# Performance work log

Hardware: AMD Instinct MI355X
Metric: run time of the kernel (lower is better)

Reference implementation:

```python
import jax, jax.numpy as jnp
import numpy as np

N = 50000      # nodes
K = 16         # neighbors per node (adj has K+1 cols; col 0 = self, sliced off)
NFEAT = 128
NHID = 128
NCLASS = 64
SLOPE = 0.2    # LeakyReLU slope used by Tail-GNN Relation module


def _relation(xg, mean_x, G1, G2, B1, B2, r):
    # xg: [N,K,F] gathered neighbor features, mean_x: [N,F] weighted mean
    # FiLM-style relation (TransE translation), mean-pooled over neighbors
    nb = (mean_x @ G2)[:, None, :]
    gamma = jax.nn.leaky_relu(jnp.einsum('nkf,fg->nkg', xg, G1) + nb, SLOPE) + 1.0
    nb2 = (mean_x @ B2)[:, None, :]
    beta = jax.nn.leaky_relu(jnp.einsum('nkf,fg->nkg', xg, B1) + nb2, SLOPE)
    r_v = gamma * r + beta                       # [N,K,F]
    return jnp.mean(xg + r_v - mean_x[:, None, :], axis=1)  # [N,F]


def _lrgcn(x, idx, w1, w2, W, G1, G2, B1, B2, r):
    nbr = idx[:, 1:]                              # [N,K] drop self column
    xg = x[nbr]                                   # [N,K,F] irregular gather
    mean_x = jnp.mean(xg * w1[:, 1:, None], axis=1)   # [N,F]
    m = _relation(xg, mean_x, G1, G2, B1, B2, r)      # [N,F]
    # tail=False branch: embed = mean_k(W(xg) * w2); W is linear (no bias)
    # so aggregate first, then transform (same math, less memory)
    embed = jnp.mean(xg * w2[:, 1:, None], axis=1) @ W  # [N,H]
    return embed, m


def setup_inputs() -> dict:
    key = jax.random.key(0)
    ks = jax.random.split(key, 20)
    s = 0.05
    inp = {
        'x': jax.random.normal(ks[0], (N, NFEAT), jnp.float32),
        'adj1_idx': jax.random.randint(ks[1], (N, K + 1), 0, N),
        'adj1_w1': jax.random.uniform(ks[2], (N, K + 1), jnp.float32),
        'adj1_w2': jax.random.uniform(ks[3], (N, K + 1), jnp.float32),
        'adj2_idx': jax.random.randint(ks[4], (N, K + 1), 0, N),
        'adj2_w1': jax.random.uniform(ks[5], (N, K + 1), jnp.float32),
        'adj2_w2': jax.random.uniform(ks[6], (N, K + 1), jnp.float32),
        'W1': jax.random.normal(ks[7], (NFEAT, NHID), jnp.float32) * s,
        'W2': jax.random.normal(ks[8], (NHID, NCLASS), jnp.float32) * s,
        'r1_G1': jax.random.normal(ks[9], (NFEAT, NFEAT), jnp.float32) * s,
        'r1_G2': jax.random.normal(ks[10], (NFEAT, NFEAT), jnp.float32) * s,
        'r1_B1': jax.random.normal(ks[11], (NFEAT, NFEAT), jnp.float32) * s,
        'r1_B2': jax.random.normal(ks[12], (NFEAT, NFEAT), jnp.float32) * s,
        'r1_r': jax.random.normal(ks[13], (NFEAT,), jnp.float32) * s,
        'r2_G1': jax.random.normal(ks[14], (NHID, NHID), jnp.float32) * s,
        'r2_G2': jax.random.normal(ks[15], (NHID, NHID), jnp.float32) * s,
        'r2_B1': jax.random.normal(ks[16], (NHID, NHID), jnp.float32) * s,
        'r2_B2': jax.random.normal(ks[17], (NHID, NHID), jnp.float32) * s,
        'r2_r': jax.random.normal(ks[18], (NHID,), jnp.float32) * s,
    }
    return inp


def reference(x, adj1_idx, adj1_w1, adj1_w2, adj2_idx, adj2_w1, adj2_w2,
              W1, W2, r1_G1, r1_G2, r1_B1, r1_B2, r1_r,
              r2_G1, r2_G2, r2_B1, r2_B2, r2_r):
    h1, m1 = _lrgcn(x, adj1_idx, adj1_w1, adj1_w2, W1,
                    r1_G1, r1_G2, r1_B1, r1_B2, r1_r)
    # eval mode: dropout is identity
    h1 = jax.nn.elu(h1)
    h2, m2 = _lrgcn(h1, adj2_idx, adj2_w1, adj2_w2, W2,
                    r2_G1, r2_G2, r2_B1, r2_B2, r2_r)
    return h2  # [N, NCLASS]
```

## Files before the change

### kernel.cpp

```cpp
#include <hip/hip_runtime.h>
#include <hip/hip_bf16.h>


#define NN   50000
#define KNBR 16
#define NF   128
#define NC   64

typedef short s16x8 __attribute__((ext_vector_type(8)));
typedef float f32x4 __attribute__((ext_vector_type(4)));

static __device__ __forceinline__ unsigned short f2bf(float f) {
  __hip_bfloat16 h = __float2bfloat16(f);
  return reinterpret_cast<unsigned short&>(h);
}
static __device__ __forceinline__ float bflo(unsigned int u) {
  return __uint_as_float(u << 16);
}
static __device__ __forceinline__ float bfhi(unsigned int u) {
  return __uint_as_float(u & 0xffff0000u);
}

template <int BN_, bool ABF16>
__global__ __launch_bounds__(256, 2) void gemm_mfma(
    const void* __restrict__ Ap, const float* __restrict__ B,
    unsigned short* __restrict__ C, int M) {
  constexpr int CT = BN_ / 16;
  constexpr int KP = 136;
  __shared__ unsigned short Wt_s[BN_ * KP];
  __shared__ unsigned short st_s[4][16 * KP];

  const int t = threadIdx.x;
  for (int i = t; i < 128 * BN_; i += 256) {
    const int k = i / BN_, c = i % BN_;
    Wt_s[c * KP + k] = f2bf(B[i]);
  }
  __syncthreads();

  const int w   = t >> 6;
  const int l   = t & 63;
  const int lr  = l & 15;
  const int lk  = l >> 4;
  const int bm0 = blockIdx.x * 128 + w * 32;

  const int row0 = bm0 + lr, row1 = row0 + 16;
  const int r0c = row0 < M ? row0 : M - 1;
  const int r1c = row1 < M ? row1 : M - 1;

  f32x4 acc[2][CT];
#pragma unroll
  for (int mt = 0; mt < 2; ++mt)
#pragma unroll
    for (int ct = 0; ct < CT; ++ct) acc[mt][ct] = (f32x4){0.f, 0.f, 0.f, 0.f};

#pragma unroll
  for (int ks = 0; ks < 4; ++ks) {
    s16x8 af[2];
    if (ABF16) {
      const uint4* A4 = reinterpret_cast<const uint4*>(Ap);
      af[0] = __builtin_bit_cast(s16x8, A4[(size_t)r0c * (NF / 8) + ks * 4 + lk]);
      af[1] = __builtin_bit_cast(s16x8, A4[(size_t)r1c * (NF / 8) + ks * 4 + lk]);
    } else {
      const float4* A4 = reinterpret_cast<const float4*>(Ap);
      const float4 u0 = A4[(size_t)r0c * 32 + ks * 8 + lk * 2];
      const float4 u1 = A4[(size_t)r0c * 32 + ks * 8 + lk * 2 + 1];
      const float4 v0 = A4[(size_t)r1c * 32 + ks * 8 + lk * 2];
      const float4 v1 = A4[(size_t)r1c * 32 + ks * 8 + lk * 2 + 1];
      unsigned short a0[8] = {f2bf(u0.x), f2bf(u0.y), f2bf(u0.z), f2bf(u0.w),
                              f2bf(u1.x), f2bf(u1.y), f2bf(u1.z), f2bf(u1.w)};
      unsigned short a1[8] = {f2bf(v0.x), f2bf(v0.y), f2bf(v0.z), f2bf(v0.w),
                              f2bf(v1.x), f2bf(v1.y), f2bf(v1.z), f2bf(v1.w)};
      af[0] = __builtin_bit_cast(s16x8, *(uint4*)a0);
      af[1] = __builtin_bit_cast(s16x8, *(uint4*)a1);
    }
    const int kb = ks * 32 + lk * 8;
#pragma unroll
    for (int ct = 0; ct < CT; ++ct) {
      const uint4 bw = *reinterpret_cast<const uint4*>(&Wt_s[(ct * 16 + lr) * KP + kb]);
      const s16x8 bf = __builtin_bit_cast(s16x8, bw);
      acc[0][ct] = __builtin_amdgcn_mfma_f32_16x16x32_bf16(af[0], bf, acc[0][ct], 0, 0, 0);
      acc[1][ct] = __builtin_amdgcn_mfma_f32_16x16x32_bf16(af[1], bf, acc[1][ct], 0, 0, 0);
    }
  }

  unsigned short* st = st_s[w];
#pragma unroll
  for (int mt = 0; mt < 2; ++mt) {
#pragma unroll
    for (int ct = 0; ct < CT; ++ct)
#pragma unroll
      for (int r = 0; r < 4; ++r)
        st[(lk * 4 + r) * KP + ct * 16 + lr] = f2bf(acc[mt][ct][r]);
    if (BN_ == 128) {
#pragma unroll
      for (int p = 0; p < 4; ++p) {
        const int ri = p * 4 + lk;
        const int grow = bm0 + mt * 16 + ri;
        if (grow < M) {
          const uint4 v = *reinterpret_cast<const uint4*>(&st[ri * KP + lr * 8]);
          *reinterpret_cast<uint4*>(&C[(size_t)grow * BN_ + lr * 8]) = v;
        }
      }
    } else {
#pragma unroll
      for (int p = 0; p < 2; ++p) {
        const int ri = p * 8 + (l >> 3);
        const int grow = bm0 + mt * 16 + ri;
        if (grow < M) {
          const uint4 v = *reinterpret_cast<const uint4*>(&st[ri * KP + (l & 7) * 8]);
          *reinterpret_cast<uint4*>(&C[(size_t)grow * BN_ + (l & 7) * 8]) = v;
        }
      }
    }
  }
}

__global__ __launch_bounds__(256) void gather_mean_128_bf16(
    const unsigned short* __restrict__ Y, const int* __restrict__ idx,
    const float* __restrict__ w, unsigned short* __restrict__ out) {
  __shared__ int   idx_s[16][KNBR];
  __shared__ float w_s[16][KNBR];
  const int t = threadIdx.x, n0 = blockIdx.x * 16;
  {
    const int node = t >> 4, k = t & 15;
    const int g = (n0 + node) * (KNBR + 1) + 1 + k;
    idx_s[node][k] = idx[g];
    w_s[node][k]   = w[g];
  }
  __syncthreads();

  const uint4* Y4 = reinterpret_cast<const uint4*>(Y);
  const int n = t >> 4, l = t & 15;
  float acc[8];
#pragma unroll
  for (int j = 0; j < 8; ++j) acc[j] = 0.f;
#pragma unroll
  for (int k = 0; k < KNBR; ++k) {
    const uint4 v  = Y4[(size_t)idx_s[n][k] * (NF / 8) + l];
    const float wv = w_s[n][k];
    acc[0] += wv * bflo(v.x); acc[1] += wv * bfhi(v.x);
    acc[2] += wv * bflo(v.y); acc[3] += wv * bfhi(v.y);
    acc[4] += wv * bflo(v.z); acc[5] += wv * bfhi(v.z);
    acc[6] += wv * bflo(v.w); acc[7] += wv * bfhi(v.w);
  }
  uint4 r;
  unsigned int* rp = &r.x;
#pragma unroll
  for (int j = 0; j < 4; ++j) {
    float a = acc[2 * j] * (1.f / KNBR);
    float b = acc[2 * j + 1] * (1.f / KNBR);
    a = a > 0.f ? a : expm1f(a);
    b = b > 0.f ? b : expm1f(b);
    rp[j] = (unsigned int)f2bf(a) | ((unsigned int)f2bf(b) << 16);
  }
  reinterpret_cast<uint4*>(out)[(size_t)(n0 + n) * (NF / 8) + l] = r;
}

__global__ __launch_bounds__(256) void gather_mean_64_bf16(
    const unsigned short* __restrict__ Y, const int* __restrict__ idx,
    const float* __restrict__ w, float* __restrict__ out) {
  __shared__ int   idx_s[16][KNBR];
  __shared__ float w_s[16][KNBR];
  const int t = threadIdx.x, n0 = blockIdx.x * 16;
  {
    const int node = t >> 4, k = t & 15;
    const int g = (n0 + node) * (KNBR + 1) + 1 + k;
    idx_s[node][k] = idx[g];
    w_s[node][k]   = w[g];
  }
  __syncthreads();

  const uint2* Y2 = reinterpret_cast<const uint2*>(Y);
  const int n = t >> 4, l = t & 15;
  float a0 = 0.f, a1 = 0.f, a2 = 0.f, a3 = 0.f;
#pragma unroll
  for (int k = 0; k < KNBR; ++k) {
    const uint2 v  = Y2[(size_t)idx_s[n][k] * (NC / 4) + l];
    const float wv = w_s[n][k];
    a0 += wv * bflo(v.x); a1 += wv * bfhi(v.x);
    a2 += wv * bflo(v.y); a3 += wv * bfhi(v.y);
  }
  reinterpret_cast<float4*>(out)[(size_t)(n0 + n) * (NC / 4) + l] = make_float4(
      a0 * (1.f / KNBR), a1 * (1.f / KNBR), a2 * (1.f / KNBR),
      a3 * (1.f / KNBR));
}

extern "C" void kernel_launch(void* const* d_in, const int* in_sizes, int n_in,
                              void* d_out, int out_size, void* d_ws,
                              size_t ws_size, hipStream_t stream) {
  const float* x   = (const float*)d_in[0];
  const int*   a1i = (const int*)d_in[1];
  const float* a1w = (const float*)d_in[3];
  const int*   a2i = (const int*)d_in[4];
  const float* a2w = (const float*)d_in[6];
  const float* W1  = (const float*)d_in[7];
  const float* W2  = (const float*)d_in[8];
  float*       out = (float*)d_out;

  unsigned short* Y1 = (unsigned short*)d_ws;
  unsigned short* h1 = Y1 + (size_t)NN * NF;
  unsigned short* Y2 = Y1;

  const int gg = (NN + 127) / 128;
  gemm_mfma<NF, false><<<gg, 256, 0, stream>>>(x, W1, Y1, NN);
  gather_mean_128_bf16<<<NN / 16, 256, 0, stream>>>(Y1, a1i, a1w, h1);
  gemm_mfma<NC, true><<<gg, 256, 0, stream>>>(h1, W2, Y2, NN);
  gather_mean_64_bf16<<<NN / 16, 256, 0, stream>>>(Y2, a2i, a2w, out);
}
```

Measured before the change: 65.10 us.

## Store GEMM outputs in column-sliced layout and gather per slice for cache locality

The GEMM epilogues now write their output in a feature-sliced layout: 8 slices, each holding 16 or 8 bf16 columns for every node contiguously. The gather kernels assign each block one slice and one range of nodes, so the random-row gathers touch a smaller working set per slice that can stay in L2/LLC. Index and weight loads are staged through shared memory using nontemporal loads. In exchange, each index and weight row is now read 8 times (once per slice), and the per-thread gathers are narrower and less coalesced.

```diff
diff --git a/kernel.cpp b/kernel.cpp
--- a/kernel.cpp
+++ b/kernel.cpp
@@ -84,6 +84,7 @@
   }
 
   unsigned short* st = st_s[w];
+  uint4* C4 = reinterpret_cast<uint4*>(C);
 #pragma unroll
   for (int mt = 0; mt < 2; ++mt) {
 #pragma unroll
@@ -98,7 +99,7 @@
         const int grow = bm0 + mt * 16 + ri;
         if (grow < M) {
           const uint4 v = *reinterpret_cast<const uint4*>(&st[ri * KP + lr * 8]);
-          *reinterpret_cast<uint4*>(&C[(size_t)grow * BN_ + lr * 8]) = v;
+          C4[((size_t)(lr >> 1) * NN + grow) * 2 + (lr & 1)] = v;
         }
       }
     } else {
@@ -108,35 +109,42 @@
         const int grow = bm0 + mt * 16 + ri;
         if (grow < M) {
           const uint4 v = *reinterpret_cast<const uint4*>(&st[ri * KP + (l & 7) * 8]);
-          *reinterpret_cast<uint4*>(&C[(size_t)grow * BN_ + (l & 7) * 8]) = v;
+          C4[(size_t)(l & 7) * NN + grow] = v;
         }
       }
     }
   }
 }
 
-__global__ __launch_bounds__(256) void gather_mean_128_bf16(
+__global__ __launch_bounds__(256) void gather_sliced_16(
     const unsigned short* __restrict__ Y, const int* __restrict__ idx,
-    const float* __restrict__ w, unsigned short* __restrict__ out) {
-  __shared__ int   idx_s[16][KNBR];
-  __shared__ float w_s[16][KNBR];
-  const int t = threadIdx.x, n0 = blockIdx.x * 16;
-  {
-    const int node = t >> 4, k = t & 15;
-    const int g = (n0 + node) * (KNBR + 1) + 1 + k;
-    idx_s[node][k] = idx[g];
-    w_s[node][k]   = w[g];
+    const float* __restrict__ w, unsigned short* __restrict__ h1) {
+  __shared__ int   idx_s[128][17];
+  __shared__ float w_s[128][17];
+  const int t = threadIdx.x;
+  const int slice = blockIdx.x & 7;
+  const int n0 = (blockIdx.x >> 3) * 128;
+#pragma unroll
+  for (int j = 0; j < 8; ++j) {
+    const int i = t + j * 256;
+    const int node = i >> 4, k = i & 15;
+    int gn = n0 + node; if (gn >= NN) gn = NN - 1;
+    const int g = gn * (KNBR + 1) + 1 + k;
+    idx_s[node][k] = __builtin_nontemporal_load(&idx[g]);
+    w_s[node][k]   = __builtin_nontemporal_load(&w[g]);
   }
   __syncthreads();
 
+  const int n = t >> 1, q = t & 1;
+  const int gn = n0 + n;
+  if (gn >= NN) return;
   const uint4* Y4 = reinterpret_cast<const uint4*>(Y);
-  const int n = t >> 4, l = t & 15;
   float acc[8];
 #pragma unroll
   for (int j = 0; j < 8; ++j) acc[j] = 0.f;
 #pragma unroll
   for (int k = 0; k < KNBR; ++k) {
-    const uint4 v  = Y4[(size_t)idx_s[n][k] * (NF / 8) + l];
+    const uint4 v  = Y4[((size_t)slice * NN + idx_s[n][k]) * 2 + q];
     const float wv = w_s[n][k];
     acc[0] += wv * bflo(v.x); acc[1] += wv * bfhi(v.x);
     acc[2] += wv * bflo(v.y); acc[3] += wv * bfhi(v.y);
@@ -153,36 +161,51 @@
     b = b > 0.f ? b : expm1f(b);
     rp[j] = (unsigned int)f2bf(a) | ((unsigned int)f2bf(b) << 16);
   }
-  reinterpret_cast<uint4*>(out)[(size_t)(n0 + n) * (NF / 8) + l] = r;
-}
-
-__global__ __launch_bounds__(256) void gather_mean_64_bf16(
+  reinterpret_cast<uint4*>(h1)[(size_t)gn * 16 + slice * 2 + q] = r;
+}
+
+__global__ __launch_bounds__(256) void gather_sliced_8(
     const unsigned short* __restrict__ Y, const int* __restrict__ idx,
     const float* __restrict__ w, float* __restrict__ out) {
-  __shared__ int   idx_s[16][KNBR];
-  __shared__ float w_s[16][KNBR];
-  const int t = threadIdx.x, n0 = blockIdx.x * 16;
-  {
-    const int node = t >> 4, k = t & 15;
-    const int g = (n0 + node) * (KNBR + 1) + 1 + k;
-    idx_s[node][k] = idx[g];
-    w_s[node][k]   = w[g];
+  __shared__ int   idx_s[256][17];
+  __shared__ float w_s[256][17];
+  const int t = threadIdx.x;
+  const int slice = blockIdx.x & 7;
+  const int n0 = (blockIdx.x >> 3) * 256;
+#pragma unroll
+  for (int j = 0; j < 16; ++j) {
+    const int i = t + j * 256;
+    const int node = i >> 4, k = i & 15;
+    int gn = n0 + node; if (gn >= NN) gn = NN - 1;
+    const int g = gn * (KNBR + 1) + 1 + k;
+    idx_s[node][k] = __builtin_nontemporal_load(&idx[g]);
+    w_s[node][k]   = __builtin_nontemporal_load(&w[g]);
   }
   __syncthreads();
 
-  const uint2* Y2 = reinterpret_cast<const uint2*>(Y);
-  const int n = t >> 4, l = t & 15;
-  float a0 = 0.f, a1 = 0.f, a2 = 0.f, a3 = 0.f;
+  const int gn = n0 + t;
+  if (gn >= NN) return;
+  const uint4* Y4 = reinterpret_cast<const uint4*>(Y);
+  float acc[8];
+#pragma unroll
+  for (int j = 0; j < 8; ++j) acc[j] = 0.f;
 #pragma unroll
   for (int k = 0; k < KNBR; ++k) {
-    const uint2 v  = Y2[(size_t)idx_s[n][k] * (NC / 4) + l];
-    const float wv = w_s[n][k];
-    a0 += wv * bflo(v.x); a1 += wv * bfhi(v.x);
-    a2 += wv * bflo(v.y); a3 += wv * bfhi(v.y);
-  }
-  reinterpret_cast<float4*>(out)[(size_t)(n0 + n) * (NC / 4) + l] = make_float4(
-      a0 * (1.f / KNBR), a1 * (1.f / KNBR), a2 * (1.f / KNBR),
-      a3 * (1.f / KNBR));
+    const uint4 v  = Y4[(size_t)slice * NN + idx_s[t][k]];
+    const float wv = w_s[t][k];
+    acc[0] += wv * bflo(v.x); acc[1] += wv * bfhi(v.x);
+    acc[2] += wv * bflo(v.y); acc[3] += wv * bfhi(v.y);
+    acc[4] += wv * bflo(v.z); acc[5] += wv * bfhi(v.z);
+    acc[6] += wv * bflo(v.w); acc[7] += wv * bfhi(v.w);
+  }
+  float4 r0 = make_float4(acc[0] * (1.f / KNBR), acc[1] * (1.f / KNBR),
+                          acc[2] * (1.f / KNBR), acc[3] * (1.f / KNBR));
+  float4 r1 = make_float4(acc[4] * (1.f / KNBR), acc[5] * (1.f / KNBR),
+                          acc[6] * (1.f / KNBR), acc[7] * (1.f / KNBR));
+  float4* o4 = reinterpret_cast<float4*>(out);
+  const size_t ob = ((size_t)gn * NC + slice * 8) >> 2;
+  o4[ob]     = r0;
+  o4[ob + 1] = r1;
 }
 
 extern "C" void kernel_launch(void* const* d_in, const int* in_sizes, int n_in,
@@ -203,7 +226,7 @@
 
   const int gg = (NN + 127) / 128;
   gemm_mfma<NF, false><<<gg, 256, 0, stream>>>(x, W1, Y1, NN);
-  gather_mean_128_bf16<<<NN / 16, 256, 0, stream>>>(Y1, a1i, a1w, h1);
+  gather_sliced_16<<<8 * 391, 256, 0, stream>>>(Y1, a1i, a1w, h1);
   gemm_mfma<NC, true><<<gg, 256, 0, stream>>>(h1, W2, Y2, NN);
-  gather_mean_64_bf16<<<NN / 16, 256, 0, stream>>>(Y2, a2i, a2w, out);
-}
+  gather_sliced_8<<<8 * 196, 256, 0, stream>>>(Y2, a2i, a2w, out);
+}
```

Result: slower. 113.0 us (+73.6%).

## Fuse layer-1 gather/ELU with layer-2 GEMM and widen gather kernels

Applied to the files above, without the earlier changes.

Merges the first neighbor gather-mean plus ELU with the second GEMM in one kernel, so h1 stays in shared memory instead of going through global memory, and one launch is removed. The gather kernels now handle 64 nodes per 512-thread block and issue all 16 neighbor loads before accumulating, which raises memory-level parallelism. The fused kernel reloads W2 into shared memory in every block and has a heavier shared-memory footprint, which may lower occupancy.

```diff
diff --git a/kernel.cpp b/kernel.cpp
--- a/kernel.cpp
+++ b/kernel.cpp
@@ -21,18 +21,17 @@
   return __uint_as_float(u & 0xffff0000u);
 }
 
-template <int BN_, bool ABF16>
-__global__ __launch_bounds__(256, 2) void gemm_mfma(
-    const void* __restrict__ Ap, const float* __restrict__ B,
+__global__ __launch_bounds__(256, 2) void gemm_mfma_128(
+    const float* __restrict__ A, const float* __restrict__ B,
     unsigned short* __restrict__ C, int M) {
-  constexpr int CT = BN_ / 16;
+  constexpr int CT = 8;
   constexpr int KP = 136;
-  __shared__ unsigned short Wt_s[BN_ * KP];
+  __shared__ unsigned short Wt_s[128 * KP];
   __shared__ unsigned short st_s[4][16 * KP];
 
   const int t = threadIdx.x;
-  for (int i = t; i < 128 * BN_; i += 256) {
-    const int k = i / BN_, c = i % BN_;
+  for (int i = t; i < 128 * 128; i += 256) {
+    const int k = i >> 7, c = i & 127;
     Wt_s[c * KP + k] = f2bf(B[i]);
   }
   __syncthreads();
@@ -53,33 +52,26 @@
 #pragma unroll
     for (int ct = 0; ct < CT; ++ct) acc[mt][ct] = (f32x4){0.f, 0.f, 0.f, 0.f};
 
+  const float4* A4 = reinterpret_cast<const float4*>(A);
 #pragma unroll
   for (int ks = 0; ks < 4; ++ks) {
-    s16x8 af[2];
-    if (ABF16) {
-      const uint4* A4 = reinterpret_cast<const uint4*>(Ap);
-      af[0] = __builtin_bit_cast(s16x8, A4[(size_t)r0c * (NF / 8) + ks * 4 + lk]);
-      af[1] = __builtin_bit_cast(s16x8, A4[(size_t)r1c * (NF / 8) + ks * 4 + lk]);
-    } else {
-      const float4* A4 = reinterpret_cast<const float4*>(Ap);
-      const float4 u0 = A4[(size_t)r0c * 32 + ks * 8 + lk * 2];
-      const float4 u1 = A4[(size_t)r0c * 32 + ks * 8 + lk * 2 + 1];
-      const float4 v0 = A4[(size_t)r1c * 32 + ks * 8 + lk * 2];
-      const float4 v1 = A4[(size_t)r1c * 32 + ks * 8 + lk * 2 + 1];
-      unsigned short a0[8] = {f2bf(u0.x), f2bf(u0.y), f2bf(u0.z), f2bf(u0.w),
-                              f2bf(u1.x), f2bf(u1.y), f2bf(u1.z), f2bf(u1.w)};
-      unsigned short a1[8] = {f2bf(v0.x), f2bf(v0.y), f2bf(v0.z), f2bf(v0.w),
-                              f2bf(v1.x), f2bf(v1.y), f2bf(v1.z), f2bf(v1.w)};
-      af[0] = __builtin_bit_cast(s16x8, *(uint4*)a0);
-      af[1] = __builtin_bit_cast(s16x8, *(uint4*)a1);
-    }
+    const float4 u0 = A4[(size_t)r0c * 32 + ks * 8 + lk * 2];
+    const float4 u1 = A4[(size_t)r0c * 32 + ks * 8 + lk * 2 + 1];
+    const float4 v0 = A4[(size_t)r1c * 32 + ks * 8 + lk * 2];
+    const float4 v1 = A4[(size_t)r1c * 32 + ks * 8 + lk * 2 + 1];
+    unsigned short a0[8] = {f2bf(u0.x), f2bf(u0.y), f2bf(u0.z), f2bf(u0.w),
+                            f2bf(u1.x), f2bf(u1.y), f2bf(u1.z), f2bf(u1.w)};
+    unsigned short a1[8] = {f2bf(v0.x), f2bf(v0.y), f2bf(v0.z), f2bf(v0.w),
+                            f2bf(v1.x), f2bf(v1.y), f2bf(v1.z), f2bf(v1.w)};
+    s16x8 af0 = __builtin_bit_cast(s16x8, *(uint4*)a0);
+    s16x8 af1 = __builtin_bit_cast(s16x8, *(uint4*)a1);
     const int kb = ks * 32 + lk * 8;
 #pragma unroll
     for (int ct = 0; ct < CT; ++ct) {
       const uint4 bw = *reinterpret_cast<const uint4*>(&Wt_s[(ct * 16 + lr) * KP + kb]);
       const s16x8 bf = __builtin_bit_cast(s16x8, bw);
-      acc[0][ct] = __builtin_amdgcn_mfma_f32_16x16x32_bf16(af[0], bf, acc[0][ct], 0, 0, 0);
-      acc[1][ct] = __builtin_amdgcn_mfma_f32_16x16x32_bf16(af[1], bf, acc[1][ct], 0, 0, 0);
+      acc[0][ct] = __builtin_amdgcn_mfma_f32_16x16x32_bf16(af0, bf, acc[0][ct], 0, 0, 0);
+      acc[1][ct] = __builtin_amdgcn_mfma_f32_16x16x32_bf16(af1, bf, acc[1][ct], 0, 0, 0);
     }
   }
 
@@ -91,98 +83,168 @@
 #pragma unroll
       for (int r = 0; r < 4; ++r)
         st[(lk * 4 + r) * KP + ct * 16 + lr] = f2bf(acc[mt][ct][r]);
-    if (BN_ == 128) {
-#pragma unroll
-      for (int p = 0; p < 4; ++p) {
-        const int ri = p * 4 + lk;
-        const int grow = bm0 + mt * 16 + ri;
-        if (grow < M) {
-          const uint4 v = *reinterpret_cast<const uint4*>(&st[ri * KP + lr * 8]);
-          *reinterpret_cast<uint4*>(&C[(size_t)grow * BN_ + lr * 8]) = v;
-        }
-      }
-    } else {
-#pragma unroll
-      for (int p = 0; p < 2; ++p) {
-        const int ri = p * 8 + (l >> 3);
-        const int grow = bm0 + mt * 16 + ri;
-        if (grow < M) {
-          const uint4 v = *reinterpret_cast<const uint4*>(&st[ri * KP + (l & 7) * 8]);
-          *reinterpret_cast<uint4*>(&C[(size_t)grow * BN_ + (l & 7) * 8]) = v;
-        }
-      }
-    }
-  }
-}
-
-__global__ __launch_bounds__(256) void gather_mean_128_bf16(
-    const unsigned short* __restrict__ Y, const int* __restrict__ idx,
-    const float* __restrict__ w, unsigned short* __restrict__ out) {
-  __shared__ int   idx_s[16][KNBR];
-  __shared__ float w_s[16][KNBR];
-  const int t = threadIdx.x, n0 = blockIdx.x * 16;
-  {
-    const int node = t >> 4, k = t & 15;
-    const int g = (n0 + node) * (KNBR + 1) + 1 + k;
+#pragma unroll
+    for (int p = 0; p < 4; ++p) {
+      const int ri = p * 4 + lk;
+      const int grow = bm0 + mt * 16 + ri;
+      if (grow < M) {
+        const uint4 v = *reinterpret_cast<const uint4*>(&st[ri * KP + lr * 8]);
+        *reinterpret_cast<uint4*>(&C[(size_t)grow * NF + lr * 8]) = v;
+      }
+    }
+  }
+}
+
+__global__ __launch_bounds__(512, 4) void gather_gemm_fused(
+    const unsigned short* __restrict__ Y1, const int* __restrict__ idx,
+    const float* __restrict__ w, const float* __restrict__ W2,
+    unsigned short* __restrict__ Y2) {
+  constexpr int KP = 136;
+  __shared__ int   idx_s[64][KNBR];
+  __shared__ float w_s[64][KNBR];
+  __shared__ unsigned short Wt_s[64 * KP];
+  __shared__ unsigned short h1_s[64 * KP];
+  __shared__ unsigned short st_s[8][16 * 40];
+
+  const int t  = threadIdx.x;
+  const int n0 = blockIdx.x * 64;
+
+#pragma unroll
+  for (int j = 0; j < 2; ++j) {
+    const int i = t + j * 512;
+    const int node = i >> 4, k = i & 15;
+    int gn = n0 + node; if (gn >= NN) gn = NN - 1;
+    const int g = gn * (KNBR + 1) + 1 + k;
     idx_s[node][k] = idx[g];
     w_s[node][k]   = w[g];
   }
-  __syncthreads();
-
-  const uint4* Y4 = reinterpret_cast<const uint4*>(Y);
-  const int n = t >> 4, l = t & 15;
-  float acc[8];
-#pragma unroll
-  for (int j = 0; j < 8; ++j) acc[j] = 0.f;
-#pragma unroll
-  for (int k = 0; k < KNBR; ++k) {
-    const uint4 v  = Y4[(size_t)idx_s[n][k] * (NF / 8) + l];
-    const float wv = w_s[n][k];
-    acc[0] += wv * bflo(v.x); acc[1] += wv * bfhi(v.x);
-    acc[2] += wv * bflo(v.y); acc[3] += wv * bfhi(v.y);
-    acc[4] += wv * bflo(v.z); acc[5] += wv * bfhi(v.z);
-    acc[6] += wv * bflo(v.w); acc[7] += wv * bfhi(v.w);
-  }
-  uint4 r;
-  unsigned int* rp = &r.x;
-#pragma unroll
-  for (int j = 0; j < 4; ++j) {
-    float a = acc[2 * j] * (1.f / KNBR);
-    float b = acc[2 * j + 1] * (1.f / KNBR);
-    a = a > 0.f ? a : expm1f(a);
-    b = b > 0.f ? b : expm1f(b);
-    rp[j] = (unsigned int)f2bf(a) | ((unsigned int)f2bf(b) << 16);
-  }
-  reinterpret_cast<uint4*>(out)[(size_t)(n0 + n) * (NF / 8) + l] = r;
-}
-
-__global__ __launch_bounds__(256) void gather_mean_64_bf16(
-    const unsigned short* __restrict__ Y, const int* __restrict__ idx,
+#pragma unroll
+  for (int j = 0; j < 16; ++j) {
+    const int i = t + j * 512;
+    const int k = i >> 6, c = i & 63;
+    Wt_s[c * KP + k] = f2bf(W2[i]);
+  }
+  __syncthreads();
+
+  const uint4* Y14 = reinterpret_cast<const uint4*>(Y1);
+  {
+    const int l = t & 15;
+#pragma unroll
+    for (int half = 0; half < 2; ++half) {
+      const int n = half * 32 + (t >> 4);
+      uint4 v[KNBR];
+#pragma unroll
+      for (int k = 0; k < KNBR; ++k)
+        v[k] = Y14[(size_t)idx_s[n][k] * 16 + l];
+      float acc[8];
+#pragma unroll
+      for (int j = 0; j < 8; ++j) acc[j] = 0.f;
+#pragma unroll
+      for (int k = 0; k < KNBR; ++k) {
+        const float wv = w_s[n][k];
+        acc[0] += wv * bflo(v[k].x); acc[1] += wv * bfhi(v[k].x);
+        acc[2] += wv * bflo(v[k].y); acc[3] += wv * bfhi(v[k].y);
+        acc[4] += wv * bflo(v[k].z); acc[5] += wv * bfhi(v[k].z);
+        acc[6] += wv * bflo(v[k].w); acc[7] += wv * bfhi(v[k].w);
+      }
+      uint4 r;
+      unsigned int* rp = &r.x;
+#pragma unroll
+      for (int j = 0; j < 4; ++j) {
+        float a = acc[2 * j] * (1.f / KNBR);
+        float b = acc[2 * j + 1] * (1.f / KNBR);
+        a = a > 0.f ? a : expm1f(a);
+        b = b > 0.f ? b : expm1f(b);
+        rp[j] = (unsigned int)f2bf(a) | ((unsigned int)f2bf(b) << 16);
+      }
+      *reinterpret_cast<uint4*>(&h1_s[n * KP + l * 8]) = r;
+    }
+  }
+  __syncthreads();
+
+  {
+    const int wv_ = t >> 6;
+    const int l   = t & 63;
+    const int lr  = l & 15;
+    const int lk  = l >> 4;
+    const int mt  = wv_ >> 1;
+    const int ch  = wv_ & 1;
+
+    f32x4 acc[2];
+    acc[0] = (f32x4){0.f, 0.f, 0.f, 0.f};
+    acc[1] = (f32x4){0.f, 0.f, 0.f, 0.f};
+#pragma unroll
+    for (int ks = 0; ks < 4; ++ks) {
+      const int kb = ks * 32 + lk * 8;
+      const uint4 aw = *reinterpret_cast<const uint4*>(&h1_s[(mt * 16 + lr) * KP + kb]);
+      const s16x8 af = __builtin_bit_cast(s16x8, aw);
+#pragma unroll
+      for (int ct = 0; ct < 2; ++ct) {
+        const uint4 bw = *reinterpret_cast<const uint4*>(
+            &Wt_s[(ch * 32 + ct * 16 + lr) * KP + kb]);
+        const s16x8 bf = __builtin_bit_cast(s16x8, bw);
+        acc[ct] = __builtin_amdgcn_mfma_f32_16x16x32_bf16(af, bf, acc[ct], 0, 0, 0);
+      }
+    }
+
+    unsigned short* st = st_s[wv_];
+#pragma unroll
+    for (int ct = 0; ct < 2; ++ct)
+#pragma unroll
+      for (int r = 0; r < 4; ++r)
+        st[(lk * 4 + r) * 40 + ct * 16 + lr] = f2bf(acc[ct][r]);
+    const int ri = l >> 2;
+    const int grow = n0 + mt * 16 + ri;
+    if (grow < NN) {
+      const uint4 v = *reinterpret_cast<const uint4*>(&st[ri * 40 + (l & 3) * 8]);
+      *reinterpret_cast<uint4*>(&Y2[(size_t)grow * NC + ch * 32 + (l & 3) * 8]) = v;
+    }
+  }
+}
+
+__global__ __launch_bounds__(512) void gather_mean_out(
+    const unsigned short* __restrict__ Y2, const int* __restrict__ idx,
     const float* __restrict__ w, float* __restrict__ out) {
-  __shared__ int   idx_s[16][KNBR];
-  __shared__ float w_s[16][KNBR];
-  const int t = threadIdx.x, n0 = blockIdx.x * 16;
-  {
-    const int node = t >> 4, k = t & 15;
-    const int g = (n0 + node) * (KNBR + 1) + 1 + k;
+  __shared__ int   idx_s[64][KNBR];
+  __shared__ float w_s[64][KNBR];
+  const int t  = threadIdx.x;
+  const int n0 = blockIdx.x * 64;
+#pragma unroll
+  for (int j = 0; j < 2; ++j) {
+    const int i = t + j * 512;
+    const int node = i >> 4, k = i & 15;
+    int gn = n0 + node; if (gn >= NN) gn = NN - 1;
+    const int g = gn * (KNBR + 1) + 1 + k;
     idx_s[node][k] = idx[g];
     w_s[node][k]   = w[g];
   }
   __syncthreads();
 
-  const uint2* Y2 = reinterpret_cast<const uint2*>(Y);
-  const int n = t >> 4, l = t & 15;
-  float a0 = 0.f, a1 = 0.f, a2 = 0.f, a3 = 0.f;
+  const int n = t >> 3, l = t & 7;
+  const int gn = n0 + n;
+  if (gn >= NN) return;
+  const uint4* Y24 = reinterpret_cast<const uint4*>(Y2);
+  uint4 v[KNBR];
+#pragma unroll
+  for (int k = 0; k < KNBR; ++k)
+    v[k] = Y24[(size_t)idx_s[n][k] * 8 + l];
+  float acc[8];
+#pragma unroll
+  for (int j = 0; j < 8; ++j) acc[j] = 0.f;
 #pragma unroll
   for (int k = 0; k < KNBR; ++k) {
-    const uint2 v  = Y2[(size_t)idx_s[n][k] * (NC / 4) + l];
     const float wv = w_s[n][k];
-    a0 += wv * bflo(v.x); a1 += wv * bfhi(v.x);
-    a2 += wv * bflo(v.y); a3 += wv * bfhi(v.y);
-  }
-  reinterpret_cast<float4*>(out)[(size_t)(n0 + n) * (NC / 4) + l] = make_float4(
-      a0 * (1.f / KNBR), a1 * (1.f / KNBR), a2 * (1.f / KNBR),
-      a3 * (1.f / KNBR));
+    acc[0] += wv * bflo(v[k].x); acc[1] += wv * bfhi(v[k].x);
+    acc[2] += wv * bflo(v[k].y); acc[3] += wv * bfhi(v[k].y);
+    acc[4] += wv * bflo(v[k].z); acc[5] += wv * bfhi(v[k].z);
+    acc[6] += wv * bflo(v[k].w); acc[7] += wv * bfhi(v[k].w);
+  }
+  float4* o4 = reinterpret_cast<float4*>(out);
+  const size_t ob = ((size_t)gn * NC + l * 8) >> 2;
+  o4[ob] = make_float4(acc[0] * (1.f / KNBR), acc[1] * (1.f / KNBR),
+                       acc[2] * (1.f / KNBR), acc[3] * (1.f / KNBR));
+  o4[ob + 1] = make_float4(acc[4] * (1.f / KNBR), acc[5] * (1.f / KNBR),
+                           acc[6] * (1.f / KNBR), acc[7] * (1.f / KNBR));
 }
 
 extern "C" void kernel_launch(void* const* d_in, const int* in_sizes, int n_in,
@@ -198,12 +260,9 @@
   float*       out = (float*)d_out;
 
   unsigned short* Y1 = (unsigned short*)d_ws;
-  unsigned short* h1 = Y1 + (size_t)NN * NF;
-  unsigned short* Y2 = Y1;
-
-  const int gg = (NN + 127) / 128;
-  gemm_mfma<NF, false><<<gg, 256, 0, stream>>>(x, W1, Y1, NN);
-  gather_mean_128_bf16<<<NN / 16, 256, 0, stream>>>(Y1, a1i, a1w, h1);
-  gemm_mfma<NC, true><<<gg, 256, 0, stream>>>(h1, W2, Y2, NN);
-  gather_mean_64_bf16<<<NN / 16, 256, 0, stream>>>(Y2, a2i, a2w, out);
-}
+  unsigned short* Y2 = Y1 + (size_t)NN * NF;
+
+  gemm_mfma_128<<<(NN + 127) / 128, 256, 0, stream>>>(x, W1, Y1, NN);
+  gather_gemm_fused<<<(NN + 63) / 64, 512, 0, stream>>>(Y1, a1i, a1w, W2, Y2);
+  gather_mean_out<<<(NN + 63) / 64, 512, 0, stream>>>(Y2, a2i, a2w, out);
+}
```

Result: faster. 58.67 us (-9.9%).
